# Performance work log

Measured on AMD Instinct MI355X. Metric: run time of the kernel, lower is better.

## Reference

```python
import jax, jax.numpy as jnp
import numpy as np

DIM = 64
N_EMBED = 512


def setup_inputs() -> dict:
    key = jax.random.key(0)
    k_x, k_e = jax.random.split(key)
    x = jax.random.normal(k_x, (32, 64, 64, DIM), dtype=jnp.float32)
    # codebook buffer: embed has shape [dim, n_embed] as in the torch module
    embed = jax.random.normal(k_e, (DIM, N_EMBED), dtype=jnp.float32)
    return {"x": x, "embed": embed}


def reference(x, embed):
    # x: [B, H, W, dim]; embed: [dim, n_embed]
    dim = embed.shape[0]
    flat = x.reshape(-1, dim)  # [N, dim]
    # squared euclidean distance (same argmin as torch.cdist's euclid dist)
    # d2[n, k] = ||flat[n]||^2 - 2 flat[n].embed[:,k] + ||embed[:,k]||^2
    d2 = (
        jnp.sum(flat * flat, axis=1, keepdims=True)
        - 2.0 * (flat @ embed)
        + jnp.sum(embed * embed, axis=0)[None, :]
    )  # [N, n_embed]
    embed_ind = jnp.argmin(d2, axis=1)  # [N]
    embed_ind = embed_ind.reshape(x.shape[:-1])  # [B, H, W]
    # embedding lookup from embed.T ([n_embed, dim])
    quantize = jnp.take(embed.T, embed_ind, axis=0)  # [B, H, W, dim]
    diff = jnp.mean(jnp.square(jax.lax.stop_gradient(quantize) - x))
    # straight-through estimator
    quantize_st = x + jax.lax.stop_gradient(quantize - x)
    return quantize_st, diff, embed_ind
```

## Files before the change

### kernel.cpp

```cpp
#include <hip/hip_runtime.h>


#define DIM      64
#define NCODE    512
#define NVEC     (32 * 64 * 64)
#define WAVES    4
#define BLK      256
#define NCT      16
#define CHUNK_DW 3072

typedef unsigned int u32;
typedef __attribute__((ext_vector_type(8)))  short bf16x8;
typedef __attribute__((ext_vector_type(16))) float f32x16;

#define GLOAD_LDS16(gp, lp)                                                      \
  __builtin_amdgcn_global_load_lds(                                              \
      (const __attribute__((address_space(1))) u32*)(gp),                        \
      (__attribute__((address_space(3))) u32*)(lp), 16, 0, 0)

__device__ __forceinline__ void split3(float v, u32& h, u32& m, u32& lo) {
    const u32 u = __float_as_uint(v);
    h = u >> 16;
    const float r1 = v - __uint_as_float(u & 0xFFFF0000u);
    const u32 u1 = __float_as_uint(r1);
    m = u1 >> 16;
    const float r2 = r1 - __uint_as_float(u1 & 0xFFFF0000u);
    lo = __float_as_uint(r2) >> 16;
}

__global__ void vq_prep(const float* __restrict__ embed,
                        u32* __restrict__ bfrag,
                        float* __restrict__ et,
                        float* __restrict__ norms) {
    const int tg = blockIdx.x * BLK + threadIdx.x;
    {
        const int ct = tg >> 6, l = tg & 63;
        const int c = ct * 32 + (l & 31), kh = l >> 5;
        double nsum = 0.0;
        u32 w[3][4][4];
        #pragma unroll
        for (int s = 0; s < 4; ++s) {
            float v[8];
            #pragma unroll
            for (int j = 0; j < 8; ++j) {
                const int d = 16 * s + kh * 8 + j;
                v[j] = embed[d * NCODE + c];
                nsum += (double)v[j] * (double)v[j];
            }
            #pragma unroll
            for (int q = 0; q < 4; ++q) {
                u32 h0, m0, l0, h1, m1, l1;
                split3(v[2 * q], h0, m0, l0);
                split3(v[2 * q + 1], h1, m1, l1);
                w[0][s][q] = h0 | (h1 << 16);
                w[1][s][q] = m0 | (m1 << 16);
                w[2][s][q] = l0 | (l1 << 16);
            }
        }
        const double tot = nsum + __shfl_xor(nsum, 32, 64);
        if (kh == 0) norms[c] = (float)tot;
        #pragma unroll
        for (int p = 0; p < 3; ++p) {
            #pragma unroll
            for (int s = 0; s < 4; ++s) {
                u32* dst = bfrag + ct * CHUNK_DW + (p * 4 + s) * 256 + l * 4;
                *reinterpret_cast<uint4*>(dst) =
                    make_uint4(w[p][s][0], w[p][s][1], w[p][s][2], w[p][s][3]);
            }
        }
    }
    {
        const int c = tg >> 1, dh = (tg & 1) * 32;
        float buf[32];
        #pragma unroll
        for (int i = 0; i < 32; ++i) buf[i] = embed[(dh + i) * NCODE + c];
        #pragma unroll
        for (int i = 0; i < 8; ++i)
            *reinterpret_cast<float4*>(et + c * DIM + dh + i * 4) =
                make_float4(buf[4 * i], buf[4 * i + 1], buf[4 * i + 2], buf[4 * i + 3]);
    }
}

__global__ __launch_bounds__(BLK, 3) void vq_main(
        const float* __restrict__ x,
        const u32* __restrict__ bfrag,
        const float* __restrict__ et,
        const float* __restrict__ norms,
        float* __restrict__ out) {
    __shared__ u32 lbuf[2][CHUNK_DW];
    __shared__ float lnorm[NCODE];
    __shared__ int sbk[WAVES][32];
    __shared__ float red[WAVES];

    const int tid = threadIdx.x;
    const int wid = tid >> 6, l = tid & 63;
    const int rl = l & 31, kh = l >> 5;
    const int n0 = (blockIdx.x * WAVES + wid) * 32;

    for (int i = tid; i < NCODE; i += BLK) lnorm[i] = norms[i];

    bf16x8 afr[3][4];
    {
        const float* xp = x + (size_t)(n0 + rl) * DIM + kh * 8;
        #pragma unroll
        for (int s = 0; s < 4; ++s) {
            const float4 va = *reinterpret_cast<const float4*>(xp + 16 * s);
            const float4 vb = *reinterpret_cast<const float4*>(xp + 16 * s + 4);
            const float v[8] = {va.x, va.y, va.z, va.w, vb.x, vb.y, vb.z, vb.w};
            #pragma unroll
            for (int q = 0; q < 4; ++q) {
                u32 h0, m0, l0, h1, m1, l1;
                split3(v[2 * q], h0, m0, l0);
                split3(v[2 * q + 1], h1, m1, l1);
                afr[0][s][2 * q] = (short)h0;  afr[0][s][2 * q + 1] = (short)h1;
                afr[1][s][2 * q] = (short)m0;  afr[1][s][2 * q + 1] = (short)m1;
                afr[2][s][2 * q] = (short)l0;  afr[2][s][2 * q + 1] = (short)l1;
            }
        }
    }

    {
        const u32* gsrc = bfrag + wid * 256 + (l << 2);
        u32* lp = &lbuf[0][wid * 256];
        #pragma unroll
        for (int i = 0; i < 3; ++i) GLOAD_LDS16(gsrc + i * 1024, lp + i * 1024);
    }
    __syncthreads();

    float best[16];
    int bk[16];
    #pragma unroll
    for (int r = 0; r < 16; ++r) { best[r] = __builtin_inff(); bk[r] = 0; }

    int cur = 0;
    for (int ct = 0; ct < NCT; ++ct) {
        if (ct + 1 < NCT) {
            const u32* gsrc = bfrag + (ct + 1) * CHUNK_DW + wid * 256 + (l << 2);
            u32* lp = &lbuf[cur ^ 1][wid * 256];
            #pragma unroll
            for (int i = 0; i < 3; ++i) GLOAD_LDS16(gsrc + i * 1024, lp + i * 1024);
        }

        f32x16 acc;
        #pragma unroll
        for (int r = 0; r < 16; ++r) acc[r] = 0.0f;

        const int l4 = l << 2;
        #pragma unroll
        for (int s = 0; s < 4; ++s) {
            const bf16x8 bh = *reinterpret_cast<const bf16x8*>(&lbuf[cur][(0 * 4 + s) * 256 + l4]);
            const bf16x8 bm = *reinterpret_cast<const bf16x8*>(&lbuf[cur][(1 * 4 + s) * 256 + l4]);
            const bf16x8 bl = *reinterpret_cast<const bf16x8*>(&lbuf[cur][(2 * 4 + s) * 256 + l4]);
            acc = __builtin_amdgcn_mfma_f32_32x32x16_bf16(afr[0][s], bh, acc, 0, 0, 0);
            acc = __builtin_amdgcn_mfma_f32_32x32x16_bf16(afr[0][s], bm, acc, 0, 0, 0);
            acc = __builtin_amdgcn_mfma_f32_32x32x16_bf16(afr[1][s], bh, acc, 0, 0, 0);
            acc = __builtin_amdgcn_mfma_f32_32x32x16_bf16(afr[1][s], bm, acc, 0, 0, 0);
            acc = __builtin_amdgcn_mfma_f32_32x32x16_bf16(afr[0][s], bl, acc, 0, 0, 0);
            acc = __builtin_amdgcn_mfma_f32_32x32x16_bf16(afr[2][s], bh, acc, 0, 0, 0);
        }

        const int col = ct * 32 + rl;
        const float nrm = lnorm[col];
        #pragma unroll
        for (int r = 0; r < 16; ++r) {
            const float sc = fmaf(-2.0f, acc[r], nrm);
            if (sc < best[r]) { best[r] = sc; bk[r] = col; }
        }

        __syncthreads();
        cur ^= 1;
    }

    #pragma unroll
    for (int off = 1; off <= 16; off <<= 1) {
        #pragma unroll
        for (int r = 0; r < 16; ++r) {
            const float ob = __shfl_xor(best[r], off, 64);
            const int obk  = __shfl_xor(bk[r], off, 64);
            if (ob < best[r] || (ob == best[r] && obk < bk[r])) { best[r] = ob; bk[r] = obk; }
        }
    }
    if (rl == 0) {
        #pragma unroll
        for (int r = 0; r < 16; ++r) sbk[wid][(r & 3) + 8 * (r >> 2) + 4 * kh] = bk[r];
    }

    float dp = 0.0f;
    const int rsub = l >> 4;
    const int dcol = (l & 15) * 4;
    #pragma unroll
    for (int i = 0; i < 8; ++i) {
        const int row = i * 4 + rsub;
        const int k = sbk[wid][row];
        const float4 q  = *reinterpret_cast<const float4*>(et + k * DIM + dcol);
        const float4 xv = *reinterpret_cast<const float4*>(x + (size_t)(n0 + row) * DIM + dcol);
        *reinterpret_cast<float4*>(out + (size_t)(n0 + row) * DIM + dcol) = q;
        const float d0 = q.x - xv.x, d1 = q.y - xv.y, d2 = q.z - xv.z, d3 = q.w - xv.w;
        dp = fmaf(d0, d0, dp); dp = fmaf(d1, d1, dp);
        dp = fmaf(d2, d2, dp); dp = fmaf(d3, d3, dp);
    }
    if (l < 32) out[(size_t)NVEC * DIM + 1 + n0 + l] = (float)sbk[wid][l];

    #pragma unroll
    for (int off = 32; off >= 1; off >>= 1) dp += __shfl_down(dp, off, 64);
    if (l == 0) red[wid] = dp;
    __syncthreads();
    if (tid == 0) {
        const float s = (red[0] + red[1]) + (red[2] + red[3]);
        atomicAdd(out + (size_t)NVEC * DIM, s * (1.0f / ((float)NVEC * (float)DIM)));
    }
}

extern "C" void kernel_launch(void* const* d_in, const int* in_sizes, int n_in,
                              void* d_out, int out_size, void* d_ws, size_t ws_size,
                              hipStream_t stream) {
    const float* x     = (const float*)d_in[0];
    const float* embed = (const float*)d_in[1];
    float* out = (float*)d_out;

    u32* bfrag   = (u32*)d_ws;
    float* et    = (float*)d_ws + NCT * CHUNK_DW;
    float* norms = et + (size_t)NCODE * DIM;

    hipMemsetAsync((char*)d_out + (size_t)NVEC * DIM * sizeof(float), 0,
                   sizeof(float), stream);

    vq_prep<<<4, BLK, 0, stream>>>(embed, bfrag, et, norms);
    vq_main<<<NVEC / (WAVES * 32), BLK, 0, stream>>>(x, bfrag, et, norms, out);
}
```

Baseline: 137.0 us.

## Fuse codebook prep into main kernel and process 64 rows per wave

Removes the separate prep kernel: each block now computes codebook norms and bf16 split fragments itself from the raw embed, staging the next chunk through registers into LDS instead of async global-to-LDS copies. Each wave now handles two 32-row groups with two accumulators, so each LDS B fragment is reused twice and fewer blocks are launched. The cost is that every block redundantly recomputes all 512 norms (a 64x512 read per block) and does split arithmetic per chunk. The final lookup also gathers strided columns from embed instead of a transposed copy.

Result: slower. 157.3 us (+14.8%).

```diff
diff --git a/kernel.cpp b/kernel.cpp
--- a/kernel.cpp
+++ b/kernel.cpp
@@ -4,19 +4,13 @@
 #define DIM      64
 #define NCODE    512
 #define NVEC     (32 * 64 * 64)
-#define WAVES    4
 #define BLK      256
 #define NCT      16
-#define CHUNK_DW 3072
+#define TILE_DW  3072
 
 typedef unsigned int u32;
 typedef __attribute__((ext_vector_type(8)))  short bf16x8;
 typedef __attribute__((ext_vector_type(16))) float f32x16;
-
-#define GLOAD_LDS16(gp, lp)                                                      \
-  __builtin_amdgcn_global_load_lds(                                              \
-      (const __attribute__((address_space(1))) u32*)(gp),                        \
-      (__attribute__((address_space(3))) u32*)(lp), 16, 0, 0)
 
 __device__ __forceinline__ void split3(float v, u32& h, u32& m, u32& lo) {
     const u32 u = __float_as_uint(v);
@@ -28,80 +22,68 @@
     lo = __float_as_uint(r2) >> 16;
 }
 
-__global__ void vq_prep(const float* __restrict__ embed,
-                        u32* __restrict__ bfrag,
-                        float* __restrict__ et,
-                        float* __restrict__ norms) {
-    const int tg = blockIdx.x * BLK + threadIdx.x;
-    {
-        const int ct = tg >> 6, l = tg & 63;
-        const int c = ct * 32 + (l & 31), kh = l >> 5;
-        double nsum = 0.0;
-        u32 w[3][4][4];
-        #pragma unroll
-        for (int s = 0; s < 4; ++s) {
-            float v[8];
-            #pragma unroll
-            for (int j = 0; j < 8; ++j) {
-                const int d = 16 * s + kh * 8 + j;
-                v[j] = embed[d * NCODE + c];
-                nsum += (double)v[j] * (double)v[j];
-            }
-            #pragma unroll
-            for (int q = 0; q < 4; ++q) {
-                u32 h0, m0, l0, h1, m1, l1;
-                split3(v[2 * q], h0, m0, l0);
-                split3(v[2 * q + 1], h1, m1, l1);
-                w[0][s][q] = h0 | (h1 << 16);
-                w[1][s][q] = m0 | (m1 << 16);
-                w[2][s][q] = l0 | (l1 << 16);
-            }
-        }
-        const double tot = nsum + __shfl_xor(nsum, 32, 64);
-        if (kh == 0) norms[c] = (float)tot;
-        #pragma unroll
-        for (int p = 0; p < 3; ++p) {
-            #pragma unroll
-            for (int s = 0; s < 4; ++s) {
-                u32* dst = bfrag + ct * CHUNK_DW + (p * 4 + s) * 256 + l * 4;
-                *reinterpret_cast<uint4*>(dst) =
-                    make_uint4(w[p][s][0], w[p][s][1], w[p][s][2], w[p][s][3]);
-            }
-        }
-    }
-    {
-        const int c = tg >> 1, dh = (tg & 1) * 32;
-        float buf[32];
-        #pragma unroll
-        for (int i = 0; i < 32; ++i) buf[i] = embed[(dh + i) * NCODE + c];
-        #pragma unroll
-        for (int i = 0; i < 8; ++i)
-            *reinterpret_cast<float4*>(et + c * DIM + dh + i * 4) =
-                make_float4(buf[4 * i], buf[4 * i + 1], buf[4 * i + 2], buf[4 * i + 3]);
-    }
-}
-
-__global__ __launch_bounds__(BLK, 3) void vq_main(
+__device__ __forceinline__ void stage_write(const float* v, u32* dst,
+                                            int ss, int lb) {
+    u32 wH[4], wM[4], wL[4];
+    #pragma unroll
+    for (int q = 0; q < 4; ++q) {
+        u32 h0, m0, l0, h1, m1, l1;
+        split3(v[2 * q],     h0, m0, l0);
+        split3(v[2 * q + 1], h1, m1, l1);
+        wH[q] = h0 | (h1 << 16);
+        wM[q] = m0 | (m1 << 16);
+        wL[q] = l0 | (l1 << 16);
+    }
+    *reinterpret_cast<uint4*>(dst + (0 * 4 + ss) * 256 + lb * 4) =
+        make_uint4(wH[0], wH[1], wH[2], wH[3]);
+    *reinterpret_cast<uint4*>(dst + (1 * 4 + ss) * 256 + lb * 4) =
+        make_uint4(wM[0], wM[1], wM[2], wM[3]);
+    *reinterpret_cast<uint4*>(dst + (2 * 4 + ss) * 256 + lb * 4) =
+        make_uint4(wL[0], wL[1], wL[2], wL[3]);
+}
+
+__global__ __launch_bounds__(BLK, 2) void vq_fused(
         const float* __restrict__ x,
-        const u32* __restrict__ bfrag,
-        const float* __restrict__ et,
-        const float* __restrict__ norms,
+        const float* __restrict__ embed,
         float* __restrict__ out) {
-    __shared__ u32 lbuf[2][CHUNK_DW];
+    __shared__ __align__(16) u32 lbuf[2][TILE_DW];
     __shared__ float lnorm[NCODE];
-    __shared__ int sbk[WAVES][32];
-    __shared__ float red[WAVES];
+    __shared__ int sbk[4][64];
+    __shared__ float red[4];
 
     const int tid = threadIdx.x;
     const int wid = tid >> 6, l = tid & 63;
     const int rl = l & 31, kh = l >> 5;
-    const int n0 = (blockIdx.x * WAVES + wid) * 32;
-
-    for (int i = tid; i < NCODE; i += BLK) lnorm[i] = norms[i];
-
-    bf16x8 afr[3][4];
+    const int n0 = (blockIdx.x * 4 + wid) * 64;
+
+    const int sc  = tid & 31;
+    const int skh = (tid >> 5) & 1;
+    const int ss  = tid >> 6;
+    const int srow = (16 * ss + 8 * skh) * NCODE + sc;
+    const int slb  = sc + 32 * skh;
+
+    float ev[8];
     {
-        const float* xp = x + (size_t)(n0 + rl) * DIM + kh * 8;
+        const float* ep = embed + srow;
+        #pragma unroll
+        for (int j = 0; j < 8; ++j) ev[j] = ep[j * NCODE];
+    }
+    {
+        double ns0 = 0.0, ns1 = 0.0;
+        #pragma unroll 8
+        for (int d = 0; d < DIM; ++d) {
+            const float a = embed[d * NCODE + tid];
+            const float b = embed[d * NCODE + tid + 256];
+            ns0 += (double)a * (double)a;
+            ns1 += (double)b * (double)b;
+        }
+        lnorm[tid]       = (float)ns0;
+        lnorm[tid + 256] = (float)ns1;
+    }
+    bf16x8 afr[2][3][4];
+    #pragma unroll
+    for (int g = 0; g < 2; ++g) {
+        const float* xp = x + (size_t)(n0 + g * 32 + rl) * DIM + kh * 8;
         #pragma unroll
         for (int s = 0; s < 4; ++s) {
             const float4 va = *reinterpret_cast<const float4*>(xp + 16 * s);
@@ -110,63 +92,69 @@
             #pragma unroll
             for (int q = 0; q < 4; ++q) {
                 u32 h0, m0, l0, h1, m1, l1;
-                split3(v[2 * q], h0, m0, l0);
+                split3(v[2 * q],     h0, m0, l0);
                 split3(v[2 * q + 1], h1, m1, l1);
-                afr[0][s][2 * q] = (short)h0;  afr[0][s][2 * q + 1] = (short)h1;
-                afr[1][s][2 * q] = (short)m0;  afr[1][s][2 * q + 1] = (short)m1;
-                afr[2][s][2 * q] = (short)l0;  afr[2][s][2 * q + 1] = (short)l1;
+                afr[g][0][s][2 * q] = (short)h0;  afr[g][0][s][2 * q + 1] = (short)h1;
+                afr[g][1][s][2 * q] = (short)m0;  afr[g][1][s][2 * q + 1] = (short)m1;
+                afr[g][2][s][2 * q] = (short)l0;  afr[g][2][s][2 * q + 1] = (short)l1;
             }
         }
     }
-
-    {
-        const u32* gsrc = bfrag + wid * 256 + (l << 2);
-        u32* lp = &lbuf[0][wid * 256];
-        #pragma unroll
-        for (int i = 0; i < 3; ++i) GLOAD_LDS16(gsrc + i * 1024, lp + i * 1024);
-    }
+    stage_write(ev, &lbuf[0][0], ss, slb);
     __syncthreads();
 
-    float best[16];
-    int bk[16];
-    #pragma unroll
-    for (int r = 0; r < 16; ++r) { best[r] = __builtin_inff(); bk[r] = 0; }
+    float best[2][16];
+    int bk[2][16];
+    #pragma unroll
+    for (int g = 0; g < 2; ++g)
+        #pragma unroll
+        for (int r = 0; r < 16; ++r) { best[g][r] = __builtin_inff(); bk[g][r] = 0; }
 
     int cur = 0;
     for (int ct = 0; ct < NCT; ++ct) {
+        float ev2[8];
         if (ct + 1 < NCT) {
-            const u32* gsrc = bfrag + (ct + 1) * CHUNK_DW + wid * 256 + (l << 2);
-            u32* lp = &lbuf[cur ^ 1][wid * 256];
-            #pragma unroll
-            for (int i = 0; i < 3; ++i) GLOAD_LDS16(gsrc + i * 1024, lp + i * 1024);
-        }
-
-        f32x16 acc;
-        #pragma unroll
-        for (int r = 0; r < 16; ++r) acc[r] = 0.0f;
-
+            const float* ep = embed + srow + (ct + 1) * 32;
+            #pragma unroll
+            for (int j = 0; j < 8; ++j) ev2[j] = ep[j * NCODE];
+        }
+
+        f32x16 acc0, acc1;
+        #pragma unroll
+        for (int r = 0; r < 16; ++r) { acc0[r] = 0.0f; acc1[r] = 0.0f; }
+
+        const u32* lb0 = &lbuf[cur][0];
         const int l4 = l << 2;
         #pragma unroll
         for (int s = 0; s < 4; ++s) {
-            const bf16x8 bh = *reinterpret_cast<const bf16x8*>(&lbuf[cur][(0 * 4 + s) * 256 + l4]);
-            const bf16x8 bm = *reinterpret_cast<const bf16x8*>(&lbuf[cur][(1 * 4 + s) * 256 + l4]);
-            const bf16x8 bl = *reinterpret_cast<const bf16x8*>(&lbuf[cur][(2 * 4 + s) * 256 + l4]);
-            acc = __builtin_amdgcn_mfma_f32_32x32x16_bf16(afr[0][s], bh, acc, 0, 0, 0);
-            acc = __builtin_amdgcn_mfma_f32_32x32x16_bf16(afr[0][s], bm, acc, 0, 0, 0);
-            acc = __builtin_amdgcn_mfma_f32_32x32x16_bf16(afr[1][s], bh, acc, 0, 0, 0);
-            acc = __builtin_amdgcn_mfma_f32_32x32x16_bf16(afr[1][s], bm, acc, 0, 0, 0);
-            acc = __builtin_amdgcn_mfma_f32_32x32x16_bf16(afr[0][s], bl, acc, 0, 0, 0);
-            acc = __builtin_amdgcn_mfma_f32_32x32x16_bf16(afr[2][s], bh, acc, 0, 0, 0);
+            const bf16x8 bh = *reinterpret_cast<const bf16x8*>(lb0 + (0 + s) * 256 + l4);
+            const bf16x8 bm = *reinterpret_cast<const bf16x8*>(lb0 + (4 + s) * 256 + l4);
+            const bf16x8 bl = *reinterpret_cast<const bf16x8*>(lb0 + (8 + s) * 256 + l4);
+            acc0 = __builtin_amdgcn_mfma_f32_32x32x16_bf16(afr[0][0][s], bh, acc0, 0, 0, 0);
+            acc1 = __builtin_amdgcn_mfma_f32_32x32x16_bf16(afr[1][0][s], bh, acc1, 0, 0, 0);
+            acc0 = __builtin_amdgcn_mfma_f32_32x32x16_bf16(afr[0][0][s], bm, acc0, 0, 0, 0);
+            acc1 = __builtin_amdgcn_mfma_f32_32x32x16_bf16(afr[1][0][s], bm, acc1, 0, 0, 0);
+            acc0 = __builtin_amdgcn_mfma_f32_32x32x16_bf16(afr[0][1][s], bh, acc0, 0, 0, 0);
+            acc1 = __builtin_amdgcn_mfma_f32_32x32x16_bf16(afr[1][1][s], bh, acc1, 0, 0, 0);
+            acc0 = __builtin_amdgcn_mfma_f32_32x32x16_bf16(afr[0][1][s], bm, acc0, 0, 0, 0);
+            acc1 = __builtin_amdgcn_mfma_f32_32x32x16_bf16(afr[1][1][s], bm, acc1, 0, 0, 0);
+            acc0 = __builtin_amdgcn_mfma_f32_32x32x16_bf16(afr[0][0][s], bl, acc0, 0, 0, 0);
+            acc1 = __builtin_amdgcn_mfma_f32_32x32x16_bf16(afr[1][0][s], bl, acc1, 0, 0, 0);
+            acc0 = __builtin_amdgcn_mfma_f32_32x32x16_bf16(afr[0][2][s], bh, acc0, 0, 0, 0);
+            acc1 = __builtin_amdgcn_mfma_f32_32x32x16_bf16(afr[1][2][s], bh, acc1, 0, 0, 0);
         }
 
         const int col = ct * 32 + rl;
         const float nrm = lnorm[col];
         #pragma unroll
         for (int r = 0; r < 16; ++r) {
-            const float sc = fmaf(-2.0f, acc[r], nrm);
-            if (sc < best[r]) { best[r] = sc; bk[r] = col; }
-        }
-
+            const float s0 = fmaf(-2.0f, acc0[r], nrm);
+            if (s0 < best[0][r]) { best[0][r] = s0; bk[0][r] = col; }
+            const float s1 = fmaf(-2.0f, acc1[r], nrm);
+            if (s1 < best[1][r]) { best[1][r] = s1; bk[1][r] = col; }
+        }
+
+        if (ct + 1 < NCT) stage_write(ev2, &lbuf[cur ^ 1][0], ss, slb);
         __syncthreads();
         cur ^= 1;
     }
@@ -174,32 +162,44 @@
     #pragma unroll
     for (int off = 1; off <= 16; off <<= 1) {
         #pragma unroll
-        for (int r = 0; r < 16; ++r) {
-            const float ob = __shfl_xor(best[r], off, 64);
-            const int obk  = __shfl_xor(bk[r], off, 64);
-            if (ob < best[r] || (ob == best[r] && obk < bk[r])) { best[r] = ob; bk[r] = obk; }
-        }
+        for (int g = 0; g < 2; ++g)
+            #pragma unroll
+            for (int r = 0; r < 16; ++r) {
+                const float ob = __shfl_xor(best[g][r], off, 64);
+                const int obk  = __shfl_xor(bk[g][r], off, 64);
+                if (ob < best[g][r] || (ob == best[g][r] && obk < bk[g][r])) {
+                    best[g][r] = ob; bk[g][r] = obk;
+                }
+            }
     }
     if (rl == 0) {
         #pragma unroll
-        for (int r = 0; r < 16; ++r) sbk[wid][(r & 3) + 8 * (r >> 2) + 4 * kh] = bk[r];
+        for (int g = 0; g < 2; ++g)
+            #pragma unroll
+            for (int r = 0; r < 16; ++r)
+                sbk[wid][g * 32 + (r & 3) + 8 * (r >> 2) + 4 * kh] = bk[g][r];
     }
 
     float dp = 0.0f;
     const int rsub = l >> 4;
     const int dcol = (l & 15) * 4;
     #pragma unroll
-    for (int i = 0; i < 8; ++i) {
+    for (int i = 0; i < 16; ++i) {
         const int row = i * 4 + rsub;
         const int k = sbk[wid][row];
-        const float4 q  = *reinterpret_cast<const float4*>(et + k * DIM + dcol);
-        const float4 xv = *reinterpret_cast<const float4*>(x + (size_t)(n0 + row) * DIM + dcol);
-        *reinterpret_cast<float4*>(out + (size_t)(n0 + row) * DIM + dcol) = q;
-        const float d0 = q.x - xv.x, d1 = q.y - xv.y, d2 = q.z - xv.z, d3 = q.w - xv.w;
+        const float q0 = embed[(dcol + 0) * NCODE + k];
+        const float q1 = embed[(dcol + 1) * NCODE + k];
+        const float q2 = embed[(dcol + 2) * NCODE + k];
+        const float q3 = embed[(dcol + 3) * NCODE + k];
+        const float4 xv = *reinterpret_cast<const float4*>(
+            x + (size_t)(n0 + row) * DIM + dcol);
+        *reinterpret_cast<float4*>(out + (size_t)(n0 + row) * DIM + dcol) =
+            make_float4(q0, q1, q2, q3);
+        const float d0 = q0 - xv.x, d1 = q1 - xv.y, d2 = q2 - xv.z, d3 = q3 - xv.w;
         dp = fmaf(d0, d0, dp); dp = fmaf(d1, d1, dp);
         dp = fmaf(d2, d2, dp); dp = fmaf(d3, d3, dp);
     }
-    if (l < 32) out[(size_t)NVEC * DIM + 1 + n0 + l] = (float)sbk[wid][l];
+    out[(size_t)NVEC * DIM + 1 + n0 + l] = (float)sbk[wid][l];
 
     #pragma unroll
     for (int off = 32; off >= 1; off >>= 1) dp += __shfl_down(dp, off, 64);
@@ -218,13 +218,8 @@
     const float* embed = (const float*)d_in[1];
     float* out = (float*)d_out;
 
-    u32* bfrag   = (u32*)d_ws;
-    float* et    = (float*)d_ws + NCT * CHUNK_DW;
-    float* norms = et + (size_t)NCODE * DIM;
-
     hipMemsetAsync((char*)d_out + (size_t)NVEC * DIM * sizeof(float), 0,
                    sizeof(float), stream);
 
-    vq_prep<<<4, BLK, 0, stream>>>(embed, bfrag, et, norms);
-    vq_main<<<NVEC / (WAVES * 32), BLK, 0, stream>>>(x, bfrag, et, norms, out);
-}
+    vq_fused<<<NVEC / 256, BLK, 0, stream>>>(x, embed, out);
+}
```
